# Performance work log

Measured on AMD Instinct MI355X. Metric: run time of the kernel, lower is better.

## Reference

```python
import jax, jax.numpy as jnp
import numpy as np

DIM = 1024
HEADS = 8
DIM_HEAD = 64
INNER = HEADS * DIM_HEAD  # 512
N_PATCHES = 256
SCALE = DIM_HEAD ** -0.5


def setup_inputs() -> dict:
    key = jax.random.key(0)
    ks = jax.random.split(key, 6)
    s = lambda fan_in: 1.0 / np.sqrt(fan_in)
    return {
        "x": jax.random.normal(ks[0], (64, N_PATCHES, DIM), dtype=jnp.float32),
        "Wq": jax.random.normal(ks[1], (DIM, INNER), dtype=jnp.float32) * s(DIM),
        "Wkv": jax.random.normal(ks[2], (DIM, 2 * INNER), dtype=jnp.float32) * s(DIM),
        "Wout": jax.random.normal(ks[3], (INNER, DIM), dtype=jnp.float32) * s(INNER),
        "bout": jax.random.normal(ks[4], (DIM,), dtype=jnp.float32) * 0.01,
        "Wspec": jax.random.normal(ks[5], (N_PATCHES, 3 * N_PATCHES), dtype=jnp.float32) * s(N_PATCHES),
    }


def reference(x, Wq, Wkv, Wout, bout, Wspec):
    b, n, d = x.shape
    # ---- spatial: single center-query attention ----
    x_center = x[:, n // 2, :]                      # [b, d]
    q = (x_center @ Wq).reshape(b, HEADS, DIM_HEAD)  # [b, h, dh]
    kv = x @ Wkv                                     # [b, n, 2*inner]
    k, v = jnp.split(kv, 2, axis=-1)
    k = k.reshape(b, n, HEADS, DIM_HEAD).transpose(0, 2, 1, 3)  # [b, h, n, dh]
    v = v.reshape(b, n, HEADS, DIM_HEAD).transpose(0, 2, 1, 3)
    logits = jnp.einsum('bhd,bhnd->bhn', q, k) * SCALE
    attn = jax.nn.softmax(logits, axis=-1)           # [b, h, n]
    out = jnp.einsum('bhn,bhnd->bhd', attn, v).reshape(b, INNER)
    # torch expands attn over n identical rows BEFORE to_out; the rows are
    # identical, so broadcasting the projected row is the same math.
    spatial = out @ Wout + bout                      # [b, d]
    spatial_out = jnp.broadcast_to(spatial[:, None, :], (b, n, d))
    # ---- spectral: attention over transposed (feature) axis ----
    x_t = x.transpose(0, 2, 1)                       # [b, d, n]
    qkv = x_t @ Wspec                                # [b, d, 3n]
    q_s, k_s, v_s = jnp.split(qkv, 3, axis=-1)       # v_s unused (as in source)
    spec_logits = jnp.einsum('bin,bjn->bij', q_s, k_s) * SCALE  # [b, d, d]
    spec_weights = jax.nn.softmax(spec_logits, axis=-1)
    return jnp.einsum('bnd,bde->bne', spatial_out, spec_weights)
```

## Files before the change

kernel.cpp:

```cpp
#include <hip/hip_runtime.h>
#include <hip/hip_bf16.h>
#include <cstdint>

typedef _Float16 f16;
typedef _Float16 half8 __attribute__((ext_vector_type(8)));
typedef float f32x4 __attribute__((ext_vector_type(4)));

#define SCALE 0.125f

#define GLL(src, dst) __builtin_amdgcn_global_load_lds( \
    (const __attribute__((address_space(1))) unsigned int*)(src), \
    (__attribute__((address_space(3))) unsigned int*)(dst), 16, 0, 0)

__global__ __launch_bounds__(256) void prep_xf(const float* __restrict__ x, f16* __restrict__ x16,
                                               f16* __restrict__ xT) {
  __shared__ f16 tile[32][33];
  int b = blockIdx.z, nt = blockIdx.y, dt = blockIdx.x;
  int c = threadIdx.x & 31, rp = threadIdx.x >> 5;
  const float* xb = x + ((size_t)b*256 + nt*32)*1024 + dt*32;
  f16* x16b = x16 + ((size_t)b*256 + nt*32)*1024 + dt*32;
#pragma unroll
  for (int p = 0; p < 4; ++p) {
    int r = p*8 + rp;
    f16 h = (f16)xb[(size_t)r*1024 + c];
    x16b[(size_t)r*1024 + c] = h;
    tile[r][c] = h;
  }
  __syncthreads();
  f16* o = xT + ((size_t)b*1024 + dt*32)*256 + nt*32;
#pragma unroll
  for (int p = 0; p < 4; ++p) { int r = p*8 + rp; o[(size_t)r*256 + c] = tile[c][r]; }
}

__global__ __launch_bounds__(256) void prep_WkvT(const float* __restrict__ W, f16* __restrict__ Wt) {
  __shared__ float tile[32][33];
  int kt = blockIdx.x, nt = blockIdx.y;
  int c = threadIdx.x & 31, rp = threadIdx.x >> 5;
#pragma unroll
  for (int p = 0; p < 4; ++p) { int r = p*8+rp; tile[r][c] = W[(size_t)(kt*32 + r)*1024 + nt*32 + c]; }
  __syncthreads();
#pragma unroll
  for (int p = 0; p < 4; ++p) { int r = p*8+rp; Wt[(size_t)(nt*32 + r)*1024 + kt*32 + c] = (f16)tile[c][r]; }
}

__global__ __launch_bounds__(256) void prep_WspecT(const float* __restrict__ W, f16* __restrict__ Wt) {
  __shared__ float tile[32][33];
  int jt = blockIdx.x, ct = blockIdx.y;
  int c = threadIdx.x & 31, rp = threadIdx.x >> 5;
#pragma unroll
  for (int p = 0; p < 4; ++p) { int r = p*8+rp; tile[r][c] = W[(size_t)(ct*32 + r)*768 + jt*32 + c]; }
  __syncthreads();
#pragma unroll
  for (int p = 0; p < 4; ++p) { int r = p*8+rp; Wt[(size_t)(jt*32 + r)*256 + ct*32 + c] = (f16)tile[c][r]; }
}

template<int KSTEPS, int AST, int BST, int CST, bool SCALEQ>
__global__ __launch_bounds__(256) void gemm128(const f16* __restrict__ Ag, const f16* __restrict__ Bg,
                                               f16* __restrict__ Cg, size_t aB, size_t bB, size_t cB) {
  __shared__ f16 As[2][128*32];
  __shared__ f16 Bs[2][128*32];
  const f16* A = Ag + (size_t)blockIdx.z*aB;
  const f16* B = Bg + (size_t)blockIdx.z*bB;
  f16* C = Cg + (size_t)blockIdx.z*cB;
  int t = threadIdx.x, lane = t & 63, wave = t >> 6;
  int l15 = lane & 15, l4 = lane >> 4;
  int wm = wave & 1, wn = wave >> 1;
  size_t m0 = (size_t)blockIdx.x*128, n0 = (size_t)blockIdx.y*128;
  float cscale = (SCALEQ && n0 < 256) ? SCALE : 1.0f;
  f32x4 acc[4][4];
#pragma unroll
  for (int i=0;i<4;++i)
#pragma unroll
    for (int j=0;j<4;++j) acc[i][j] = (f32x4){0.f,0.f,0.f,0.f};
  int rowS[2], chS[2];
#pragma unroll
  for (int c=0;c<2;++c) {
    int slot = c*256 + t;
    rowS[c] = slot >> 2;
    chS[c]  = (slot & 3) ^ ((slot >> 3) & 3);
  }
  int pc = (l4 ^ ((l15 >> 1) & 3)) * 8;

  auto STAGE = [&](int buf, int ks) {
    int k0 = ks*32;
#pragma unroll
    for (int c=0;c<2;++c) {
      GLL(A + (m0 + rowS[c])*(size_t)AST + k0 + chS[c]*8, &As[buf][(c*256 + wave*64)*8]);
      GLL(B + (n0 + rowS[c])*(size_t)BST + k0 + chS[c]*8, &Bs[buf][(c*256 + wave*64)*8]);
    }
  };

  STAGE(0, 0);
#pragma unroll 2
  for (int ks = 0; ks < KSTEPS; ++ks) {
    int cur = ks & 1;
    if (ks + 1 < KSTEPS) {
      STAGE(cur ^ 1, ks + 1);
      asm volatile("s_waitcnt vmcnt(4)" ::: "memory");
    } else {
      asm volatile("s_waitcnt vmcnt(0)" ::: "memory");
    }
    __builtin_amdgcn_s_barrier();
    __builtin_amdgcn_sched_barrier(0);
    half8 a[4], bb[4];
    const f16* Af = &As[cur][(wm*64 + l15)*32 + pc];
    const f16* Bf = &Bs[cur][(wn*64 + l15)*32 + pc];
#pragma unroll
    for (int mi=0;mi<4;++mi) a[mi]  = *(const half8*)(Af + mi*16*32);
#pragma unroll
    for (int ni=0;ni<4;++ni) bb[ni] = *(const half8*)(Bf + ni*16*32);
    __builtin_amdgcn_s_setprio(1);
#pragma unroll
    for (int mi=0;mi<4;++mi)
#pragma unroll
      for (int ni=0;ni<4;++ni)
        acc[mi][ni] = __builtin_amdgcn_mfma_f32_16x16x32_f16(a[mi], bb[ni], acc[mi][ni], 0,0,0);
    __builtin_amdgcn_s_setprio(0);
    __builtin_amdgcn_sched_barrier(0);
    __builtin_amdgcn_s_barrier();
  }
#pragma unroll
  for (int mi=0;mi<4;++mi)
#pragma unroll
    for (int ni=0;ni<4;++ni)
#pragma unroll
      for (int j=0;j<4;++j) {
        size_t row = m0 + wm*64 + mi*16 + 4*l4 + j;
        size_t col = n0 + wn*64 + ni*16 + l15;
        C[row*CST + col] = (f16)(acc[mi][ni][j] * cscale);
      }
}

__global__ __launch_bounds__(256) void qattn(const float* __restrict__ x, const float* __restrict__ Wq,
                                             const f16* __restrict__ kv, float* __restrict__ attnout) {
  int b = blockIdx.x, h = blockIdx.y;
  int t = threadIdx.x;
  __shared__ float xc[1024];
  __shared__ float qh[64];
  __shared__ float p[256];
  __shared__ float part[4][64];
  __shared__ float redw[4];
  const float* xcg = x + ((size_t)b*256 + 128)*1024;
#pragma unroll
  for (int i = 0; i < 4; ++i) xc[t + 256*i] = xcg[t + 256*i];
  __syncthreads();
  int d = t & 63, chunk = t >> 6;
  {
    float s = 0.f;
    const float* wq = Wq + (size_t)(chunk*256)*512 + h*64 + d;
#pragma unroll 8
    for (int c = 0; c < 256; ++c) s += xc[chunk*256 + c] * wq[(size_t)c*512];
    part[chunk][d] = s;
  }
  __syncthreads();
  if (t < 64) qh[t] = part[0][t]+part[1][t]+part[2][t]+part[3][t];
  __syncthreads();
  {
    const f16* kp = kv + ((size_t)b*256 + t)*1024 + h*64;
    float acc = 0.f;
#pragma unroll
    for (int d8 = 0; d8 < 8; ++d8) {
      half8 kk = *(const half8*)(kp + d8*8);
#pragma unroll
      for (int j = 0; j < 8; ++j) acc += (float)kk[j] * qh[d8*8+j];
    }
    p[t] = acc * SCALE;
  }
  __syncthreads();
  int lane = t & 63, wid = t >> 6;
  float v = p[t];
#pragma unroll
  for (int o = 32; o >= 1; o >>= 1) v = fmaxf(v, __shfl_xor(v, o));
  if (lane == 0) redw[wid] = v;
  __syncthreads();
  float m = fmaxf(fmaxf(redw[0],redw[1]),fmaxf(redw[2],redw[3]));
  float e = __expf(p[t] - m);
  __syncthreads();
  v = e;
#pragma unroll
  for (int o = 32; o >= 1; o >>= 1) v += __shfl_xor(v, o);
  if (lane == 0) redw[wid] = v;
  __syncthreads();
  float Z = redw[0]+redw[1]+redw[2]+redw[3];
  p[t] = e / Z;
  __syncthreads();
  {
    float o = 0.f;
    const f16* vp = kv + ((size_t)b*256 + chunk*64)*1024 + 512 + h*64 + d;
#pragma unroll 8
    for (int n = 0; n < 64; ++n) o += p[chunk*64 + n] * (float)vp[(size_t)n*1024];
    part[chunk][d] = o;
  }
  __syncthreads();
  if (t < 64) attnout[(size_t)b*512 + h*64 + t] = part[0][t]+part[1][t]+part[2][t]+part[3][t];
}

__global__ __launch_bounds__(256) void spatialp(const float* __restrict__ attnout, const float* __restrict__ Wout,
                                                float* __restrict__ partial) {
  int ic = blockIdx.x, b = blockIdx.y;
  int t = threadIdx.x;
  __shared__ float ao[128];
  if (t < 128) ao[t] = attnout[(size_t)b*512 + ic*128 + t];
  __syncthreads();
  const float* W = Wout + (size_t)ic*128*1024 + t*4;
  f32x4 acc0 = (f32x4){0.f,0.f,0.f,0.f};
  f32x4 acc1 = (f32x4){0.f,0.f,0.f,0.f};
#pragma unroll 4
  for (int i = 0; i < 128; i += 2) {
    f32x4 w0 = *(const f32x4*)(W + (size_t)i*1024);
    f32x4 w1 = *(const f32x4*)(W + (size_t)(i+1)*1024);
    float a0 = ao[i], a1 = ao[i+1];
    acc0[0] += a0*w0[0]; acc0[1] += a0*w0[1]; acc0[2] += a0*w0[2]; acc0[3] += a0*w0[3];
    acc1[0] += a1*w1[0]; acc1[1] += a1*w1[1]; acc1[2] += a1*w1[2]; acc1[3] += a1*w1[3];
  }
  f32x4 acc;
#pragma unroll
  for (int j=0;j<4;++j) acc[j] = acc0[j] + acc1[j];
  *(f32x4*)(partial + ((size_t)(b*4 + ic))*1024 + t*4) = acc;
}

__global__ __launch_bounds__(256) void spatialr(const float* __restrict__ partial, const float* __restrict__ bout,
                                                float* __restrict__ spatial) {
  int b = blockIdx.x, t = threadIdx.x;
  f32x4 s = *(const f32x4*)(bout + t*4);
#pragma unroll
  for (int ic = 0; ic < 4; ++ic) {
    f32x4 p = *(const f32x4*)(partial + ((size_t)(b*4 + ic))*1024 + t*4);
#pragma unroll
    for (int j=0;j<4;++j) s[j] += p[j];
  }
  *(f32x4*)(spatial + (size_t)b*1024 + t*4) = s;
}

__global__ __launch_bounds__(512) void speck(const f16* __restrict__ qks, const float* __restrict__ spatial,
                                             float* __restrict__ r) {
  __shared__ f16 Bs[2][1024*32];
  __shared__ f16 As[2][64*32];
  __shared__ __attribute__((aligned(16))) float sz[64*8];
  int bid = blockIdx.x;
  int xcd = bid & 7, q = bid >> 3;
  int b = xcd*8 + (q >> 4);
  int iblk = q & 15;
  int t = threadIdx.x, lane = t & 63, wave = t >> 6;
  int l15 = lane & 15, l4 = lane >> 4;
  int ew = wave;
  const f16* qs = qks + (size_t)b*1024*512;
  int i0 = iblk*64;

  f32x4 acc[4][8];
#pragma unroll
  for (int rt=0;rt<4;++rt)
#pragma unroll
    for (int ct=0;ct<8;++ct) acc[rt][ct] = (f32x4){0.f,0.f,0.f,0.f};
  int pc = (l4 ^ ((l15 >> 1) & 3)) * 8;

  auto STAGE = [&](int buf, int ks) {
    int k0 = ks*32;
#pragma unroll
    for (int c = 0; c < 8; ++c) {
      int slot = c*512 + t;
      int row = slot >> 2;
      int ch = (slot & 3) ^ ((slot >> 3) & 3);
      GLL(qs + 256 + (size_t)row*512 + k0 + ch*8, &Bs[buf][(c*512 + wave*64)*8]);
    }
    {
      int w3 = wave & 3;
      int slot = w3*64 + lane;
      int row = slot >> 2;
      int ch = (slot & 3) ^ ((slot >> 3) & 3);
      GLL(qs + (size_t)(i0 + row)*512 + k0 + ch*8, &As[buf][(w3*64)*8]);
    }
  };

  STAGE(0, 0);
  for (int ks = 0; ks < 8; ++ks) {
    int cur = ks & 1;
    if (ks < 7) {
      STAGE(cur ^ 1, ks + 1);
      asm volatile("s_waitcnt vmcnt(9)" ::: "memory");
    } else {
      asm volatile("s_waitcnt vmcnt(0)" ::: "memory");
    }
    __builtin_amdgcn_s_barrier();
    __builtin_amdgcn_sched_barrier(0);
    half8 a[4];
#pragma unroll
    for (int rt = 0; rt < 4; ++rt) a[rt] = *(const half8*)(&As[cur][(rt*16 + l15)*32 + pc]);
    __builtin_amdgcn_s_setprio(1);
#pragma unroll
    for (int ct = 0; ct < 8; ++ct) {
      half8 bb = *(const half8*)(&Bs[cur][(ew*128 + ct*16 + l15)*32 + pc]);
#pragma unroll
      for (int rt = 0; rt < 4; ++rt)
        acc[rt][ct] = __builtin_amdgcn_mfma_f32_16x16x32_f16(a[rt], bb, acc[rt][ct], 0,0,0);
    }
    __builtin_amdgcn_s_setprio(0);
    __builtin_amdgcn_sched_barrier(0);
    __builtin_amdgcn_s_barrier();
  }
  float zr[4][4];
#pragma unroll
  for (int rt=0;rt<4;++rt)
#pragma unroll
    for (int jj=0;jj<4;++jj) {
      float zz = 0.f;
#pragma unroll
      for (int ct=0;ct<8;++ct) {
        float e = __expf(acc[rt][ct][jj]);
        acc[rt][ct][jj] = e;
        zz += e;
      }
#pragma unroll
      for (int o=1;o<16;o<<=1) zz += __shfl_xor(zz, o);
      zr[rt][jj] = zz;
    }
  if (l15 == 0) {
#pragma unroll
    for (int rt=0;rt<4;++rt)
#pragma unroll
      for (int jj=0;jj<4;++jj) sz[(rt*16 + 4*l4 + jj)*8 + wave] = zr[rt][jj];
  }
  __syncthreads();
  float f[4][4];
#pragma unroll
  for (int rt=0;rt<4;++rt)
#pragma unroll
    for (int jj=0;jj<4;++jj) {
      int row = rt*16 + 4*l4 + jj;
      f32x4 lo = *(const f32x4*)(&sz[row*8]);
      f32x4 hi = *(const f32x4*)(&sz[row*8+4]);
      float zz = (lo[0]+lo[1]+lo[2]+lo[3]) + (hi[0]+hi[1]+hi[2]+hi[3]);
      f[rt][jj] = spatial[(size_t)b*1024 + i0 + row] / zz;
    }
  float* rb = r + (size_t)b*1024;
#pragma unroll
  for (int ct=0;ct<8;++ct) {
    float v = 0.f;
#pragma unroll
    for (int rt=0;rt<4;++rt)
#pragma unroll
      for (int jj=0;jj<4;++jj) v += f[rt][jj]*acc[rt][ct][jj];
    v += __shfl_xor(v, 16);
    v += __shfl_xor(v, 32);
    if (l4 == 0) atomicAdd(rb + ew*128 + ct*16 + l15, v);
  }
}

__global__ __launch_bounds__(256) void bcast(const float* __restrict__ r, float* __restrict__ out) {
  size_t row = blockIdx.x;
  int b = (int)(row >> 8);
  f32x4 v = *(const f32x4*)(r + (size_t)b*1024 + threadIdx.x*4);
  *(f32x4*)(out + row*1024 + (size_t)threadIdx.x*4) = v;
}

extern "C" void kernel_launch(void* const* d_in, const int* in_sizes, int n_in,
                              void* d_out, int out_size, void* d_ws, size_t ws_size,
                              hipStream_t stream) {
  const float* x     = (const float*)d_in[0];
  const float* Wq    = (const float*)d_in[1];
  const float* Wkv   = (const float*)d_in[2];
  const float* Wout  = (const float*)d_in[3];
  const float* bout  = (const float*)d_in[4];
  const float* Wspec = (const float*)d_in[5];
  float* out = (float*)d_out;
  char* ws = (char*)d_ws;
  f16*  qks     = (f16*)(ws);
  f16*  kv      = (f16*)(ws);
  float* partial = (float*)(ws);
  f16*  x16     = (f16*)(ws + 33554432);
  f16*  xT      = (f16*)(ws + 67108864);
  f16*  WkvT    = (f16*)(ws + 100663296);
  f16*  WspecT  = (f16*)(ws + 102760448);
  float* attnout = (float*)(ws + 103022592);
  float* spatial = (float*)(ws + 103153664);
  float* rvec    = (float*)(ws + 103415808);
  (void)in_sizes; (void)n_in; (void)out_size; (void)ws_size;

  prep_xf    <<<dim3(32, 8, 64), dim3(256), 0, stream>>>(x, x16, xT);
  prep_WkvT  <<<dim3(32, 32),    dim3(256), 0, stream>>>(Wkv, WkvT);
  prep_WspecT<<<dim3(16, 8),     dim3(256), 0, stream>>>(Wspec, WspecT);
  gemm128<32,1024,1024,1024,false><<<dim3(128, 8, 1), dim3(256), 0, stream>>>(x16, WkvT, kv, 0, 0, 0);
  qattn      <<<dim3(64, 8),     dim3(256), 0, stream>>>(x, Wq, kv, attnout);
  spatialp   <<<dim3(4, 64),     dim3(256), 0, stream>>>(attnout, Wout, partial);
  spatialr   <<<dim3(64),        dim3(256), 0, stream>>>(partial, bout, spatial);
  gemm128<8,256,256,512,true><<<dim3(8, 4, 64), dim3(256), 0, stream>>>(xT, WspecT, qks,
                                                                   (size_t)1024*256, 0, (size_t)1024*512);
  hipMemsetAsync(rvec, 0, 64*1024*sizeof(float), stream);
  speck      <<<dim3(1024),      dim3(512), 0, stream>>>(qks, spatial, rvec);
  bcast      <<<dim3(16384),     dim3(256), 0, stream>>>(rvec, out);
}
```

Measured before the change: 236.8 us.

## Halve spectral tile rows and split column staging into two halves for occupancy

The spectral softmax kernel now processes 32 query rows per block instead of 64 and stages the 1024 key columns in two 512-column halves per k-step, doubling the grid to 2048 blocks. LDS per block and accumulator registers are halved, and launch bounds request 4 blocks per CU, so more waves can be resident and latency is better hidden. In exchange, every key tile is reloaded twice as many times across blocks, the pipeline has twice as many barrier-separated steps, and there are twice as many atomic adds into the result vector.

```diff
diff --git a/kernel.cpp b/kernel.cpp
--- a/kernel.cpp
+++ b/kernel.cpp
@@ -232,75 +232,74 @@
   *(f32x4*)(spatial + (size_t)b*1024 + t*4) = s;
 }
 
-__global__ __launch_bounds__(512) void speck(const f16* __restrict__ qks, const float* __restrict__ spatial,
-                                             float* __restrict__ r) {
-  __shared__ f16 Bs[2][1024*32];
-  __shared__ f16 As[2][64*32];
-  __shared__ __attribute__((aligned(16))) float sz[64*8];
+__global__ __launch_bounds__(512, 4) void speck(const f16* __restrict__ qks, const float* __restrict__ spatial,
+                                                float* __restrict__ r) {
+  __shared__ f16 Bs[2][512*32];
+  __shared__ f16 As[2][32*32];
+  __shared__ __attribute__((aligned(16))) float sz[32*8];
   int bid = blockIdx.x;
   int xcd = bid & 7, q = bid >> 3;
-  int b = xcd*8 + (q >> 4);
-  int iblk = q & 15;
+  int b = xcd*8 + (q >> 5);
+  int iblk = q & 31;
   int t = threadIdx.x, lane = t & 63, wave = t >> 6;
   int l15 = lane & 15, l4 = lane >> 4;
   int ew = wave;
   const f16* qs = qks + (size_t)b*1024*512;
-  int i0 = iblk*64;
-
-  f32x4 acc[4][8];
-#pragma unroll
-  for (int rt=0;rt<4;++rt)
+  int i0 = iblk*32;
+
+  f32x4 acc[2][8];
+#pragma unroll
+  for (int rt=0;rt<2;++rt)
 #pragma unroll
     for (int ct=0;ct<8;++ct) acc[rt][ct] = (f32x4){0.f,0.f,0.f,0.f};
   int pc = (l4 ^ ((l15 >> 1) & 3)) * 8;
 
-  auto STAGE = [&](int buf, int ks) {
+  auto STAGE = [&](int buf, int p) {
+    int ks = p >> 1, h = p & 1;
     int k0 = ks*32;
 #pragma unroll
-    for (int c = 0; c < 8; ++c) {
+    for (int c = 0; c < 4; ++c) {
       int slot = c*512 + t;
       int row = slot >> 2;
       int ch = (slot & 3) ^ ((slot >> 3) & 3);
-      GLL(qs + 256 + (size_t)row*512 + k0 + ch*8, &Bs[buf][(c*512 + wave*64)*8]);
+      GLL(qs + (size_t)(512*h + row)*512 + 256 + k0 + ch*8, &Bs[buf][(c*512 + wave*64)*8]);
     }
     {
-      int w3 = wave & 3;
-      int slot = w3*64 + lane;
+      int slot = ((wave & 1) << 6) + lane;
       int row = slot >> 2;
       int ch = (slot & 3) ^ ((slot >> 3) & 3);
-      GLL(qs + (size_t)(i0 + row)*512 + k0 + ch*8, &As[buf][(w3*64)*8]);
+      GLL(qs + (size_t)(i0 + row)*512 + k0 + ch*8, &As[buf][(((wave & 1) << 6))*8]);
     }
   };
 
   STAGE(0, 0);
-  for (int ks = 0; ks < 8; ++ks) {
-    int cur = ks & 1;
-    if (ks < 7) {
-      STAGE(cur ^ 1, ks + 1);
-      asm volatile("s_waitcnt vmcnt(9)" ::: "memory");
+#pragma unroll
+  for (int p = 0; p < 16; ++p) {
+    int buf = p & 1, h = p & 1;
+    if (p < 15) {
+      STAGE(buf ^ 1, p + 1);
+      asm volatile("s_waitcnt vmcnt(5)" ::: "memory");
     } else {
       asm volatile("s_waitcnt vmcnt(0)" ::: "memory");
     }
     __builtin_amdgcn_s_barrier();
     __builtin_amdgcn_sched_barrier(0);
-    half8 a[4];
-#pragma unroll
-    for (int rt = 0; rt < 4; ++rt) a[rt] = *(const half8*)(&As[cur][(rt*16 + l15)*32 + pc]);
+    half8 a0 = *(const half8*)(&As[buf][(l15)*32 + pc]);
+    half8 a1 = *(const half8*)(&As[buf][(16 + l15)*32 + pc]);
     __builtin_amdgcn_s_setprio(1);
 #pragma unroll
-    for (int ct = 0; ct < 8; ++ct) {
-      half8 bb = *(const half8*)(&Bs[cur][(ew*128 + ct*16 + l15)*32 + pc]);
-#pragma unroll
-      for (int rt = 0; rt < 4; ++rt)
-        acc[rt][ct] = __builtin_amdgcn_mfma_f32_16x16x32_f16(a[rt], bb, acc[rt][ct], 0,0,0);
+    for (int c4 = 0; c4 < 4; ++c4) {
+      half8 bb = *(const half8*)(&Bs[buf][(ew*64 + c4*16 + l15)*32 + pc]);
+      acc[0][h*4+c4] = __builtin_amdgcn_mfma_f32_16x16x32_f16(a0, bb, acc[0][h*4+c4], 0,0,0);
+      acc[1][h*4+c4] = __builtin_amdgcn_mfma_f32_16x16x32_f16(a1, bb, acc[1][h*4+c4], 0,0,0);
     }
     __builtin_amdgcn_s_setprio(0);
     __builtin_amdgcn_sched_barrier(0);
     __builtin_amdgcn_s_barrier();
   }
-  float zr[4][4];
-#pragma unroll
-  for (int rt=0;rt<4;++rt)
+  float zr[2][4];
+#pragma unroll
+  for (int rt=0;rt<2;++rt)
 #pragma unroll
     for (int jj=0;jj<4;++jj) {
       float zz = 0.f;
@@ -316,14 +315,14 @@
     }
   if (l15 == 0) {
 #pragma unroll
-    for (int rt=0;rt<4;++rt)
+    for (int rt=0;rt<2;++rt)
 #pragma unroll
       for (int jj=0;jj<4;++jj) sz[(rt*16 + 4*l4 + jj)*8 + wave] = zr[rt][jj];
   }
   __syncthreads();
-  float f[4][4];
-#pragma unroll
-  for (int rt=0;rt<4;++rt)
+  float f[2][4];
+#pragma unroll
+  for (int rt=0;rt<2;++rt)
 #pragma unroll
     for (int jj=0;jj<4;++jj) {
       int row = rt*16 + 4*l4 + jj;
@@ -337,12 +336,15 @@
   for (int ct=0;ct<8;++ct) {
     float v = 0.f;
 #pragma unroll
-    for (int rt=0;rt<4;++rt)
+    for (int rt=0;rt<2;++rt)
 #pragma unroll
       for (int jj=0;jj<4;++jj) v += f[rt][jj]*acc[rt][ct][jj];
     v += __shfl_xor(v, 16);
     v += __shfl_xor(v, 32);
-    if (l4 == 0) atomicAdd(rb + ew*128 + ct*16 + l15, v);
+    if (l4 == 0) {
+      int e = (ct < 4) ? (ew*64 + ct*16 + l15) : (512 + ew*64 + (ct-4)*16 + l15);
+      atomicAdd(rb + e, v);
+    }
   }
 }
 
@@ -386,6 +388,6 @@
   gemm128<8,256,256,512,true><<<dim3(8, 4, 64), dim3(256), 0, stream>>>(xT, WspecT, qks,
                                                                    (size_t)1024*256, 0, (size_t)1024*512);
   hipMemsetAsync(rvec, 0, 64*1024*sizeof(float), stream);
-  speck      <<<dim3(1024),      dim3(512), 0, stream>>>(qks, spatial, rvec);
+  speck      <<<dim3(2048),      dim3(512), 0, stream>>>(qks, spatial, rvec);
   bcast      <<<dim3(16384),     dim3(256), 0, stream>>>(rvec, out);
 }
```

New measurement: 252.0 us. 6.4% more time.

## Double speck workgroup to 1024 threads, halving per-wave column tiles

Applied to the files above, without the earlier changes.

The spectral-attention kernel now launches 16 waves per block instead of 8. Each wave covers 64 key columns rather than 128, so the accumulator array drops from 4x8 to 4x4 tiles. Staging loads are spread over more threads, the per-wave wait counts are adjusted, and the spatial values are preloaded into shared memory. The softmax denominator is reduced across waves with an extra shuffle step. The aim is more latency hiding and lower register pressure, at the cost of more barrier participants and a heavier cross-wave reduction.

```diff
diff --git a/kernel.cpp b/kernel.cpp
--- a/kernel.cpp
+++ b/kernel.cpp
@@ -232,52 +232,55 @@
   *(f32x4*)(spatial + (size_t)b*1024 + t*4) = s;
 }
 
-__global__ __launch_bounds__(512) void speck(const f16* __restrict__ qks, const float* __restrict__ spatial,
-                                             float* __restrict__ r) {
+__global__ __launch_bounds__(1024, 4) void speck(const f16* __restrict__ qks, const float* __restrict__ spatial,
+                                                 float* __restrict__ r) {
   __shared__ f16 Bs[2][1024*32];
   __shared__ f16 As[2][64*32];
-  __shared__ __attribute__((aligned(16))) float sz[64*8];
+  __shared__ __attribute__((aligned(16))) float sz[64*16];
+  __shared__ float zfin[64];
+  __shared__ float spat[64];
   int bid = blockIdx.x;
   int xcd = bid & 7, q = bid >> 3;
   int b = xcd*8 + (q >> 4);
   int iblk = q & 15;
   int t = threadIdx.x, lane = t & 63, wave = t >> 6;
   int l15 = lane & 15, l4 = lane >> 4;
-  int ew = wave;
   const f16* qs = qks + (size_t)b*1024*512;
   int i0 = iblk*64;
-
-  f32x4 acc[4][8];
-#pragma unroll
-  for (int rt=0;rt<4;++rt)
-#pragma unroll
-    for (int ct=0;ct<8;++ct) acc[rt][ct] = (f32x4){0.f,0.f,0.f,0.f};
+  if (t < 64) spat[t] = spatial[(size_t)b*1024 + i0 + t];
+
+  f32x4 acc[4][4];
+#pragma unroll
+  for (int mi=0;mi<4;++mi)
+#pragma unroll
+    for (int ni=0;ni<4;++ni) acc[mi][ni] = (f32x4){0.f,0.f,0.f,0.f};
   int pc = (l4 ^ ((l15 >> 1) & 3)) * 8;
 
   auto STAGE = [&](int buf, int ks) {
     int k0 = ks*32;
 #pragma unroll
-    for (int c = 0; c < 8; ++c) {
-      int slot = c*512 + t;
+    for (int c = 0; c < 4; ++c) {
+      int slot = c*1024 + t;
       int row = slot >> 2;
       int ch = (slot & 3) ^ ((slot >> 3) & 3);
-      GLL(qs + 256 + (size_t)row*512 + k0 + ch*8, &Bs[buf][(c*512 + wave*64)*8]);
-    }
-    {
-      int w3 = wave & 3;
-      int slot = w3*64 + lane;
+      GLL(qs + (size_t)row*512 + 256 + k0 + ch*8, &Bs[buf][(c*1024 + wave*64)*8]);
+    }
+    if (wave < 4) {
+      int slot = wave*64 + lane;
       int row = slot >> 2;
       int ch = (slot & 3) ^ ((slot >> 3) & 3);
-      GLL(qs + (size_t)(i0 + row)*512 + k0 + ch*8, &As[buf][(w3*64)*8]);
+      GLL(qs + (size_t)(i0 + row)*512 + k0 + ch*8, &As[buf][(wave*64)*8]);
     }
   };
 
   STAGE(0, 0);
-  for (int ks = 0; ks < 8; ++ks) {
-    int cur = ks & 1;
-    if (ks < 7) {
-      STAGE(cur ^ 1, ks + 1);
-      asm volatile("s_waitcnt vmcnt(9)" ::: "memory");
+#pragma unroll
+  for (int p = 0; p < 8; ++p) {
+    int buf = p & 1;
+    if (p < 7) {
+      STAGE(buf ^ 1, p + 1);
+      if (wave < 4) asm volatile("s_waitcnt vmcnt(5)" ::: "memory");
+      else          asm volatile("s_waitcnt vmcnt(4)" ::: "memory");
     } else {
       asm volatile("s_waitcnt vmcnt(0)" ::: "memory");
     }
@@ -285,64 +288,61 @@
     __builtin_amdgcn_sched_barrier(0);
     half8 a[4];
 #pragma unroll
-    for (int rt = 0; rt < 4; ++rt) a[rt] = *(const half8*)(&As[cur][(rt*16 + l15)*32 + pc]);
+    for (int mi = 0; mi < 4; ++mi) a[mi] = *(const half8*)(&As[buf][(mi*16 + l15)*32 + pc]);
     __builtin_amdgcn_s_setprio(1);
 #pragma unroll
-    for (int ct = 0; ct < 8; ++ct) {
-      half8 bb = *(const half8*)(&Bs[cur][(ew*128 + ct*16 + l15)*32 + pc]);
-#pragma unroll
-      for (int rt = 0; rt < 4; ++rt)
-        acc[rt][ct] = __builtin_amdgcn_mfma_f32_16x16x32_f16(a[rt], bb, acc[rt][ct], 0,0,0);
+    for (int ni = 0; ni < 4; ++ni) {
+      half8 bb = *(const half8*)(&Bs[buf][(wave*64 + ni*16 + l15)*32 + pc]);
+#pragma unroll
+      for (int mi = 0; mi < 4; ++mi)
+        acc[mi][ni] = __builtin_amdgcn_mfma_f32_16x16x32_f16(a[mi], bb, acc[mi][ni], 0,0,0);
     }
     __builtin_amdgcn_s_setprio(0);
     __builtin_amdgcn_sched_barrier(0);
     __builtin_amdgcn_s_barrier();
   }
-  float zr[4][4];
-#pragma unroll
-  for (int rt=0;rt<4;++rt)
+#pragma unroll
+  for (int mi=0;mi<4;++mi)
 #pragma unroll
     for (int jj=0;jj<4;++jj) {
-      float zz = 0.f;
-#pragma unroll
-      for (int ct=0;ct<8;++ct) {
-        float e = __expf(acc[rt][ct][jj]);
-        acc[rt][ct][jj] = e;
-        zz += e;
+      float s = 0.f;
+#pragma unroll
+      for (int ni=0;ni<4;++ni) {
+        float e = __expf(acc[mi][ni][jj]);
+        acc[mi][ni][jj] = e;
+        s += e;
       }
 #pragma unroll
-      for (int o=1;o<16;o<<=1) zz += __shfl_xor(zz, o);
-      zr[rt][jj] = zz;
-    }
-  if (l15 == 0) {
-#pragma unroll
-    for (int rt=0;rt<4;++rt)
-#pragma unroll
-      for (int jj=0;jj<4;++jj) sz[(rt*16 + 4*l4 + jj)*8 + wave] = zr[rt][jj];
+      for (int o=1;o<16;o<<=1) s += __shfl_xor(s, o);
+      if (l15 == 0) sz[(mi*16 + 4*l4 + jj)*16 + wave] = s;
+    }
+  __syncthreads();
+  {
+    float v = sz[t];
+#pragma unroll
+    for (int o=1;o<16;o<<=1) v += __shfl_xor(v, o);
+    if ((t & 15) == 0) zfin[t >> 4] = v;
   }
   __syncthreads();
   float f[4][4];
 #pragma unroll
-  for (int rt=0;rt<4;++rt)
+  for (int mi=0;mi<4;++mi)
 #pragma unroll
     for (int jj=0;jj<4;++jj) {
-      int row = rt*16 + 4*l4 + jj;
-      f32x4 lo = *(const f32x4*)(&sz[row*8]);
-      f32x4 hi = *(const f32x4*)(&sz[row*8+4]);
-      float zz = (lo[0]+lo[1]+lo[2]+lo[3]) + (hi[0]+hi[1]+hi[2]+hi[3]);
-      f[rt][jj] = spatial[(size_t)b*1024 + i0 + row] / zz;
+      int row = mi*16 + 4*l4 + jj;
+      f[mi][jj] = spat[row] / zfin[row];
     }
   float* rb = r + (size_t)b*1024;
 #pragma unroll
-  for (int ct=0;ct<8;++ct) {
+  for (int ni=0;ni<4;++ni) {
     float v = 0.f;
 #pragma unroll
-    for (int rt=0;rt<4;++rt)
-#pragma unroll
-      for (int jj=0;jj<4;++jj) v += f[rt][jj]*acc[rt][ct][jj];
+    for (int mi=0;mi<4;++mi)
+#pragma unroll
+      for (int jj=0;jj<4;++jj) v += f[mi][jj]*acc[mi][ni][jj];
     v += __shfl_xor(v, 16);
     v += __shfl_xor(v, 32);
-    if (l4 == 0) atomicAdd(rb + ew*128 + ct*16 + l15, v);
+    if (l4 == 0) atomicAdd(rb + wave*64 + ni*16 + l15, v);
   }
 }
 
@@ -386,6 +386,6 @@
   gemm128<8,256,256,512,true><<<dim3(8, 4, 64), dim3(256), 0, stream>>>(xT, WspecT, qks,
                                                                    (size_t)1024*256, 0, (size_t)1024*512);
   hipMemsetAsync(rvec, 0, 64*1024*sizeof(float), stream);
-  speck      <<<dim3(1024),      dim3(512), 0, stream>>>(qks, spatial, rvec);
+  speck      <<<dim3(1024),      dim3(1024), 0, stream>>>(qks, spatial, rvec);
   bcast      <<<dim3(16384),     dim3(256), 0, stream>>>(rvec, out);
 }
```

New measurement: 239.4 us. No clear change (+1.1%).
